# Kernel tuning notes

Measured on AMD Instinct MI355X. Metric: run time of the kernel, lower is better.

The kernel has to match this reference:

```python
import jax, jax.numpy as jnp
import numpy as np

HIDDEN = 512
BATCH = 64
SEQ = 1024
FUTURE = 16


def setup_inputs() -> dict:
    key = jax.random.key(0)
    ks = jax.random.split(key, 12)
    s = 0.05  # small init to keep the un-squashed LSTM recurrence stable
    H = HIDDEN
    inp = {
        "x": jax.random.normal(ks[0], (BATCH, SEQ), dtype=jnp.float32),
        # cell 1: input_length=1
        "W1": jax.random.normal(ks[1], (4 * H, 1), dtype=jnp.float32) * s,
        "bW1": jax.random.normal(ks[2], (4 * H,), dtype=jnp.float32) * s,
        "U1": jax.random.normal(ks[3], (4 * H, H), dtype=jnp.float32) * s,
        "bU1": jax.random.normal(ks[4], (4 * H,), dtype=jnp.float32) * s,
        # cell 2: input_length=H
        "W2": jax.random.normal(ks[5], (4 * H, H), dtype=jnp.float32) * s,
        "bW2": jax.random.normal(ks[6], (4 * H,), dtype=jnp.float32) * s,
        "U2": jax.random.normal(ks[7], (4 * H, H), dtype=jnp.float32) * s,
        "bU2": jax.random.normal(ks[8], (4 * H,), dtype=jnp.float32) * s,
        # output head: Linear(H, 1)
        "lw": jax.random.normal(ks[9], (1, H), dtype=jnp.float32) * s,
        "lb": jax.random.normal(ks[10], (1,), dtype=jnp.float32) * s,
        "future": FUTURE,
    }
    return inp


def _cell(x_t, h, c, W, bW, U, bU):
    # NOTE: faithful to source — NO sigmoid/tanh on the gates, only tanh on c_t.
    gates = x_t @ W.T + bW + h @ U.T + bU            # [B, 4H]
    i_t, f_t, g_t, o_t = jnp.split(gates, 4, axis=-1)
    c_t = f_t * c + i_t * g_t
    h_t = o_t * jnp.tanh(c_t)
    return h_t, c_t


def reference(x, W1, bW1, U1, bU1, W2, bW2, U2, bU2, lw, lb, future):
    B = x.shape[0]
    H = U1.shape[1]
    zeros = jnp.zeros((B, H), dtype=x.dtype)
    init = (zeros, zeros, zeros, zeros, jnp.zeros((B, 1), dtype=x.dtype))

    def run(carry, x_t):
        h1, c1, h2, c2, _ = carry
        h1, c1 = _cell(x_t, h1, c1, W1, bW1, U1, bU1)
        h2, c2 = _cell(h1, h2, c2, W2, bW2, U2, bU2)
        out = h2 @ lw.T + lb                          # [B, 1]
        return (h1, c1, h2, c2, out), out

    # teacher-forced pass over the observed sequence
    xs = x.T[:, :, None]                              # [T, B, 1]
    carry, outs = jax.lax.scan(run, init, xs)         # outs: [T, B, 1]

    if future > 0:
        def run_future(carry, _):
            return run(carry, carry[4])
        carry, outs_f = jax.lax.scan(run_future, carry, None, length=future)
        outs = jnp.concatenate([outs, outs_f], axis=0)

    return outs[:, :, 0].T                            # [B, T+future]
```

## Files before the change

kernel.cpp:

```cpp
#include <hip/hip_runtime.h>
#include <math.h>

#define HID 512
#define B 64
#define SEQT 1024
#define FUT 16
#define TT (SEQT + FUT)
#define NWG 256
#define TPB 512
#define NWAVE 8
#define JPW 2
#define HB (HID * B)
#define BLOBF 12288

#define WS_H1_F   512
#define WS_H2_F   (WS_H1_F + 2 * HB)
#define WS_BLOB_F (WS_H2_F + 2 * HB)
#define WS_XT_F   (WS_BLOB_F + NWG * BLOBF)
#define WS_TOT_F  (WS_XT_F + SEQT * B)

__device__ inline void pub_store(float* p, float v) {
  __hip_atomic_store(p, v, __ATOMIC_RELAXED, __HIP_MEMORY_SCOPE_AGENT);
}

__device__ inline void gbar4(int* bb, int wg, int bar) {
  __builtin_amdgcn_s_waitcnt(0);
  __syncthreads();
  const int tid  = threadIdx.x;
  const int lane = tid & 63;
  if (tid == 0) {
    __hip_atomic_store(bb + wg, bar, __ATOMIC_RELAXED, __HIP_MEMORY_SCOPE_AGENT);
    __builtin_amdgcn_fence(__ATOMIC_ACQUIRE, "agent");
  }
  if (wg == NWG - 1 && tid < 64) {
    for (;;) {
      int a = __hip_atomic_load(bb + lane,       __ATOMIC_RELAXED, __HIP_MEMORY_SCOPE_AGENT);
      int b = __hip_atomic_load(bb + 64  + lane, __ATOMIC_RELAXED, __HIP_MEMORY_SCOPE_AGENT);
      int c = __hip_atomic_load(bb + 128 + lane, __ATOMIC_RELAXED, __HIP_MEMORY_SCOPE_AGENT);
      int d = __hip_atomic_load(bb + 192 + lane, __ATOMIC_RELAXED, __HIP_MEMORY_SCOPE_AGENT);
      if (__all(a >= bar && b >= bar && c >= bar && d >= bar)) break;
      __builtin_amdgcn_s_sleep(2);
    }
    if (lane == 0)
      __hip_atomic_store(bb + 320, bar, __ATOMIC_RELAXED, __HIP_MEMORY_SCOPE_AGENT);
  }
  if (tid == 0) {
    while (__hip_atomic_load(bb + 320, __ATOMIC_RELAXED,
                             __HIP_MEMORY_SCOPE_AGENT) < bar) {
      __builtin_amdgcn_s_sleep(2);
    }
  }
  __syncthreads();
}

__global__ void __launch_bounds__(256) prep_ws(
    const float* __restrict__ x,
    const float* __restrict__ U1, const float* __restrict__ W2,
    const float* __restrict__ U2, float* __restrict__ ws)
{
  const int idx = blockIdx.x * blockDim.x + threadIdx.x;
  if (idx < WS_BLOB_F) {
    ws[idx] = 0.0f;
  }
  {
    const int i2 = idx - WS_BLOB_F;
    if (i2 >= 0 && i2 < NWG * BLOBF) {
      const int wg  = i2 / BLOBF;
      const int off = i2 - wg * BLOBF;
      const int j0  = wg * JPW;
      float v;
      if (off < 4096) {
        const int k = off >> 3, r = off & 7;
        const int row = (r >> 1) * HID + j0 + (r & 1);
        v = U1[(size_t)row * HID + k];
      } else {
        const int o2 = off - 4096;
        const int k = o2 >> 4, rr = o2 & 15;
        const int r = rr & 7;
        const int row = (r >> 1) * HID + j0 + (r & 1);
        v = (rr < 8) ? W2[(size_t)row * HID + k] : U2[(size_t)row * HID + k];
      }
      ws[WS_BLOB_F + i2] = v;
    }
  }
  {
    const int i3 = idx - WS_XT_F;
    if (i3 >= 0 && i3 < SEQT * B) {
      const int t = i3 >> 6, b = i3 & 63;
      ws[WS_XT_F + i3] = x[(size_t)b * SEQT + t];
    }
  }
}

__global__ void __launch_bounds__(TPB, 1) rnn_main(
    const float* __restrict__ W1, const float* __restrict__ bW1,
    const float* __restrict__ bU1,
    const float* __restrict__ bW2, const float* __restrict__ bU2,
    const float* __restrict__ lw, const float* __restrict__ lb,
    float* __restrict__ out,
    int* __restrict__ bb,
    float* __restrict__ h1b, float* __restrict__ h2b,
    const float* __restrict__ wbl, const float* __restrict__ xT)
{
  __shared__ float wlds[BLOBF];
  __shared__ float red[NWAVE][8][B];
  __shared__ float outred[NWAVE][B];
  __shared__ float c1s[JPW][B], c2s[JPW][B];
  __shared__ float w1c[8], bs1[8], bs2[8];

  const int wg   = blockIdx.x;
  const int j0   = wg * JPW;
  const int tid  = threadIdx.x;
  const int lane = tid & 63;
  const int wvu  = __builtin_amdgcn_readfirstlane(tid >> 6);

  {
    const float4* gsrc = (const float4*)(wbl + (size_t)wg * BLOBF);
    float4* ldst = (float4*)wlds;
    #pragma unroll
    for (int i = 0; i < BLOBF / 4 / TPB; ++i)
      ldst[i * TPB + tid] = gsrc[i * TPB + tid];
  }
  if (tid < JPW * B) { c1s[tid >> 6][lane] = 0.f; c2s[tid >> 6][lane] = 0.f; }
  if (tid < 8) {
    const int g = tid >> 1, jl = tid & 1;
    const int row = g * HID + j0 + jl;
    w1c[tid] = W1[row];
    bs1[tid] = bW1[row] + bU1[row];
    bs2[tid] = bW2[row] + bU2[row];
  }
  __syncthreads();

  const float* wl1 = wlds + wvu * 512;
  const float* wl2 = wlds + 4096 + wvu * 1024;
  const float lbv = lb[0];

  int bar = 0;
  for (int t = 0; t < TT; ++t) {
    const float* h1old = h1b + ((t + 1) & 1) * HB;
    float*       h1new = h1b + (t & 1) * HB;
    const float* h2old = h2b + ((t + 1) & 1) * HB;
    float*       h2new = h2b + (t & 1) * HB;

    float xvpref = 0.f;
    if (tid < JPW * B && t < SEQT) xvpref = xT[(size_t)t * B + lane];

    {
      const float4* hp = (const float4*)h1old + (size_t)(wvu * 16) * B + lane;
      float4 hq[16];
      #pragma unroll
      for (int i = 0; i < 16; ++i) hq[i] = hp[i * B];
      float a[8] = {0.f,0.f,0.f,0.f,0.f,0.f,0.f,0.f};
      #pragma unroll
      for (int c = 0; c < 16; ++c) {
        const float hh[4] = {hq[c].x, hq[c].y, hq[c].z, hq[c].w};
        #pragma unroll
        for (int j = 0; j < 4; ++j) {
          const float4 wA = *(const float4*)(wl1 + c * 32 + j * 8);
          const float4 wB = *(const float4*)(wl1 + c * 32 + j * 8 + 4);
          const float h = hh[j];
          a[0] = fmaf(wA.x, h, a[0]); a[1] = fmaf(wA.y, h, a[1]);
          a[2] = fmaf(wA.z, h, a[2]); a[3] = fmaf(wA.w, h, a[3]);
          a[4] = fmaf(wB.x, h, a[4]); a[5] = fmaf(wB.y, h, a[5]);
          a[6] = fmaf(wB.z, h, a[6]); a[7] = fmaf(wB.w, h, a[7]);
        }
      }
      #pragma unroll
      for (int r = 0; r < 8; ++r) red[wvu][r][lane] = a[r];
    }
    __syncthreads();

    if (tid < JPW * B) {
      const int jl = tid >> 6, b = tid & 63;
      const float xv = (t < SEQT) ? xvpref : out[(size_t)b * TT + (t - 1)];
      float gate[4];
      #pragma unroll
      for (int g = 0; g < 4; ++g) {
        const int r = g * 2 + jl;
        float s = bs1[r] + xv * w1c[r];
        #pragma unroll
        for (int w = 0; w < NWAVE; ++w) s += red[w][r][b];
        gate[g] = s;
      }
      const float c = gate[1] * c1s[jl][b] + gate[0] * gate[2];
      c1s[jl][b] = c;
      const int j = j0 + jl;
      pub_store(&h1new[(size_t)(j >> 2) * (B * 4) + b * 4 + (j & 3)],
                gate[3] * tanhf(c));
    }

    ++bar;
    gbar4(bb, wg, bar);

    if (wg == (t & 127) && t >= 1 && t <= SEQT - 1) {
      const float4* hb2 = (const float4*)h2old + (size_t)(wvu * 16) * B + lane;
      const float4* lw4 = (const float4*)lw + wvu * 16;
      float p = 0.f;
      #pragma unroll
      for (int i = 0; i < 16; ++i) {
        const float4 hv = hb2[i * B];
        const float4 wv = lw4[i];
        p = fmaf(wv.x, hv.x, p); p = fmaf(wv.y, hv.y, p);
        p = fmaf(wv.z, hv.z, p); p = fmaf(wv.w, hv.w, p);
      }
      outred[wvu][lane] = p;
      __syncthreads();
      if (tid < B) {
        float o = lbv;
        #pragma unroll
        for (int s = 0; s < NWAVE; ++s) o += outred[s][tid];
        pub_store(&out[(size_t)tid * TT + (t - 1)], o);
      }
      __syncthreads();
    }

    {
      const float4* pp4 = (const float4*)h1new + (size_t)(wvu * 16) * B + lane;
      const float4* qq4 = (const float4*)h2old + (size_t)(wvu * 16) * B + lane;
      float4 P[16], Q[16];
      #pragma unroll
      for (int i = 0; i < 16; ++i) P[i] = pp4[i * B];
      #pragma unroll
      for (int i = 0; i < 16; ++i) Q[i] = qq4[i * B];
      float a[8] = {0.f,0.f,0.f,0.f,0.f,0.f,0.f,0.f};
      #pragma unroll
      for (int c = 0; c < 16; ++c) {
        const float hp_[4] = {P[c].x, P[c].y, P[c].z, P[c].w};
        const float hq_[4] = {Q[c].x, Q[c].y, Q[c].z, Q[c].w};
        #pragma unroll
        for (int j = 0; j < 4; ++j) {
          const float4 w0 = *(const float4*)(wl2 + c * 64 + j * 16);
          const float4 w1 = *(const float4*)(wl2 + c * 64 + j * 16 + 4);
          const float4 w2 = *(const float4*)(wl2 + c * 64 + j * 16 + 8);
          const float4 w3 = *(const float4*)(wl2 + c * 64 + j * 16 + 12);
          const float hp1 = hp_[j], hq1 = hq_[j];
          a[0] = fmaf(w0.x, hp1, a[0]); a[1] = fmaf(w0.y, hp1, a[1]);
          a[2] = fmaf(w0.z, hp1, a[2]); a[3] = fmaf(w0.w, hp1, a[3]);
          a[4] = fmaf(w1.x, hp1, a[4]); a[5] = fmaf(w1.y, hp1, a[5]);
          a[6] = fmaf(w1.z, hp1, a[6]); a[7] = fmaf(w1.w, hp1, a[7]);
          a[0] = fmaf(w2.x, hq1, a[0]); a[1] = fmaf(w2.y, hq1, a[1]);
          a[2] = fmaf(w2.z, hq1, a[2]); a[3] = fmaf(w2.w, hq1, a[3]);
          a[4] = fmaf(w3.x, hq1, a[4]); a[5] = fmaf(w3.y, hq1, a[5]);
          a[6] = fmaf(w3.z, hq1, a[6]); a[7] = fmaf(w3.w, hq1, a[7]);
        }
      }
      #pragma unroll
      for (int r = 0; r < 8; ++r) red[wvu][r][lane] = a[r];
    }
    __syncthreads();

    if (tid < JPW * B) {
      const int jl = tid >> 6, b = tid & 63;
      float gate[4];
      #pragma unroll
      for (int g = 0; g < 4; ++g) {
        const int r = g * 2 + jl;
        float s = bs2[r];
        #pragma unroll
        for (int w = 0; w < NWAVE; ++w) s += red[w][r][b];
        gate[g] = s;
      }
      const float c = gate[1] * c2s[jl][b] + gate[0] * gate[2];
      c2s[jl][b] = c;
      const int j = j0 + jl;
      pub_store(&h2new[(size_t)(j >> 2) * (B * 4) + b * 4 + (j & 3)],
                gate[3] * tanhf(c));
    }
    __syncthreads();

    if (t >= SEQT - 1) {
      ++bar;
      gbar4(bb, wg, bar);
      if (wg == 0) {
        const float4* hb2 = (const float4*)h2new + (size_t)(wvu * 16) * B + lane;
        const float4* lw4 = (const float4*)lw + wvu * 16;
        float p = 0.f;
        #pragma unroll
        for (int i = 0; i < 16; ++i) {
          const float4 hv = hb2[i * B];
          const float4 wv = lw4[i];
          p = fmaf(wv.x, hv.x, p); p = fmaf(wv.y, hv.y, p);
          p = fmaf(wv.z, hv.z, p); p = fmaf(wv.w, hv.w, p);
        }
        outred[wvu][lane] = p;
        __syncthreads();
        if (tid < B) {
          float o = lbv;
          #pragma unroll
          for (int s = 0; s < NWAVE; ++s) o += outred[s][tid];
          pub_store(&out[(size_t)tid * TT + t], o);
        }
        __syncthreads();
      }
      ++bar;
      gbar4(bb, wg, bar);
    }
  }
}

__device__ inline void gbar(int* cnt, int target) {
  __syncthreads();
  if (threadIdx.x == 0) {
    __threadfence();
    __hip_atomic_fetch_add(cnt, 1, __ATOMIC_RELEASE, __HIP_MEMORY_SCOPE_AGENT);
    while (__hip_atomic_load(cnt, __ATOMIC_ACQUIRE, __HIP_MEMORY_SCOPE_AGENT) < target) {
      __builtin_amdgcn_s_sleep(2);
    }
  }
  __syncthreads();
}

__global__ void __launch_bounds__(TPB) zero_ws(float* ws, int n) {
  int i = blockIdx.x * blockDim.x + threadIdx.x;
  if (i < n) ws[i] = 0.0f;
}

__global__ void __launch_bounds__(TPB) rnn_fallback(
    const float* __restrict__ x,
    const float* __restrict__ W1, const float* __restrict__ bW1,
    const float* __restrict__ U1, const float* __restrict__ bU1,
    const float* __restrict__ W2, const float* __restrict__ bW2,
    const float* __restrict__ U2, const float* __restrict__ bU2,
    const float* __restrict__ lw, const float* __restrict__ lb,
    float* out, float* ws)
{
  __shared__ float red[NWAVE][8][B];
  __shared__ float outred[NWAVE][B];
  __shared__ float c1s[JPW][B], c2s[JPW][B];
  __shared__ float w1c[8], bs1[8], bs2[8];

  int* cnt   = (int*)ws;
  float* h1b = ws + 16;
  float* h2b = h1b + 2 * HB;

  const int wg   = blockIdx.x;
  const int j0   = wg * JPW;
  const int tid  = threadIdx.x;
  const int lane = tid & 63;
  const int wvu  = __builtin_amdgcn_readfirstlane(tid >> 6);
  const int kb   = wvu << 6;

  if (tid < JPW * B) { c1s[tid >> 6][lane] = 0.f; c2s[tid >> 6][lane] = 0.f; }
  if (tid < 8) {
    const int g = tid >> 1, jl = tid & 1;
    const int row = g * HID + j0 + jl;
    w1c[tid] = W1[row];
    bs1[tid] = bW1[row] + bU1[row];
    bs2[tid] = bW2[row] + bU2[row];
  }
  __syncthreads();

  const float* u1p[8]; const float* w2p[8]; const float* u2p[8];
  #pragma unroll
  for (int r = 0; r < 8; ++r) {
    const int row = (r >> 1) * HID + j0 + (r & 1);
    u1p[r] = U1 + (size_t)row * HID + kb;
    w2p[r] = W2 + (size_t)row * HID + kb;
    u2p[r] = U2 + (size_t)row * HID + kb;
  }
  const float lbv = lb[0];

  int bar = 0;
  for (int t = 0; t < TT; ++t) {
    const float* h1old = h1b + ((t + 1) & 1) * HB;
    float*       h1new = h1b + (t & 1) * HB;
    const float* h2old = h2b + ((t + 1) & 1) * HB;
    float*       h2new = h2b + (t & 1) * HB;

    {
      const float* hp = h1old + (size_t)kb * B;
      float a0=0.f,a1=0.f,a2=0.f,a3=0.f,a4=0.f,a5=0.f,a6=0.f,a7=0.f;
      #pragma unroll 8
      for (int k = 0; k < 64; ++k) {
        const float hv = hp[k * B + lane];
        a0 = fmaf(u1p[0][k], hv, a0); a1 = fmaf(u1p[1][k], hv, a1);
        a2 = fmaf(u1p[2][k], hv, a2); a3 = fmaf(u1p[3][k], hv, a3);
        a4 = fmaf(u1p[4][k], hv, a4); a5 = fmaf(u1p[5][k], hv, a5);
        a6 = fmaf(u1p[6][k], hv, a6); a7 = fmaf(u1p[7][k], hv, a7);
      }
      red[wvu][0][lane]=a0; red[wvu][1][lane]=a1; red[wvu][2][lane]=a2; red[wvu][3][lane]=a3;
      red[wvu][4][lane]=a4; red[wvu][5][lane]=a5; red[wvu][6][lane]=a6; red[wvu][7][lane]=a7;
    }
    __syncthreads();

    if (tid < JPW * B) {
      const int jl = tid >> 6, b = tid & 63;
      const float xv = (t < SEQT) ? x[(size_t)b * SEQT + t]
                                  : out[(size_t)b * TT + (t - 1)];
      float gate[4];
      #pragma unroll
      for (int g = 0; g < 4; ++g) {
        const int r = g * 2 + jl;
        float s = bs1[r] + xv * w1c[r];
        #pragma unroll
        for (int w = 0; w < NWAVE; ++w) s += red[w][r][b];
        gate[g] = s;
      }
      const float c = gate[1] * c1s[jl][b] + gate[0] * gate[2];
      c1s[jl][b] = c;
      h1new[(size_t)(j0 + jl) * B + b] = gate[3] * tanhf(c);
    }

    ++bar;
    gbar(cnt, NWG * bar);

    if (wg == 0 && t >= 1 && t <= SEQT - 1) {
      const float* hb2 = h2old + (size_t)(wvu * 64) * B;
      const float* lwp = lw + wvu * 64;
      float p = 0.f;
      #pragma unroll 8
      for (int j = 0; j < 64; ++j) p = fmaf(lwp[j], hb2[j * B + lane], p);
      outred[wvu][lane] = p;
      __syncthreads();
      if (tid < B) {
        float o = lbv;
        #pragma unroll
        for (int s = 0; s < NWAVE; ++s) o += outred[s][tid];
        out[(size_t)tid * TT + (t - 1)] = o;
      }
      __syncthreads();
    }

    {
      const float* h1p = h1new + (size_t)kb * B;
      const float* h2p = h2old + (size_t)kb * B;
      float s0=0.f,s1=0.f,s2=0.f,s3=0.f,s4=0.f,s5=0.f,s6=0.f,s7=0.f;
      float q0=0.f,q1=0.f,q2=0.f,q3=0.f,q4=0.f,q5=0.f,q6=0.f,q7=0.f;
      #pragma unroll 4
      for (int k = 0; k < 64; ++k) {
        const float h1v = h1p[k * B + lane];
        const float h2v = h2p[k * B + lane];
        s0 = fmaf(w2p[0][k], h1v, s0); q0 = fmaf(u2p[0][k], h2v, q0);
        s1 = fmaf(w2p[1][k], h1v, s1); q1 = fmaf(u2p[1][k], h2v, q1);
        s2 = fmaf(w2p[2][k], h1v, s2); q2 = fmaf(u2p[2][k], h2v, q2);
        s3 = fmaf(w2p[3][k], h1v, s3); q3 = fmaf(u2p[3][k], h2v, q3);
        s4 = fmaf(w2p[4][k], h1v, s4); q4 = fmaf(u2p[4][k], h2v, q4);
        s5 = fmaf(w2p[5][k], h1v, s5); q5 = fmaf(u2p[5][k], h2v, q5);
        s6 = fmaf(w2p[6][k], h1v, s6); q6 = fmaf(u2p[6][k], h2v, q6);
        s7 = fmaf(w2p[7][k], h1v, s7); q7 = fmaf(u2p[7][k], h2v, q7);
      }
      red[wvu][0][lane]=s0+q0; red[wvu][1][lane]=s1+q1;
      red[wvu][2][lane]=s2+q2; red[wvu][3][lane]=s3+q3;
      red[wvu][4][lane]=s4+q4; red[wvu][5][lane]=s5+q5;
      red[wvu][6][lane]=s6+q6; red[wvu][7][lane]=s7+q7;
    }
    __syncthreads();

    if (tid < JPW * B) {
      const int jl = tid >> 6, b = tid & 63;
      float gate[4];
      #pragma unroll
      for (int g = 0; g < 4; ++g) {
        const int r = g * 2 + jl;
        float s = bs2[r];
        #pragma unroll
        for (int w = 0; w < NWAVE; ++w) s += red[w][r][b];
        gate[g] = s;
      }
      const float c = gate[1] * c2s[jl][b] + gate[0] * gate[2];
      c2s[jl][b] = c;
      h2new[(size_t)(j0 + jl) * B + b] = gate[3] * tanhf(c);
    }
    __syncthreads();

    if (t >= SEQT - 1) {
      ++bar;
      gbar(cnt, NWG * bar);
      if (wg == 0) {
        const float* hb2 = h2new + (size_t)(wvu * 64) * B;
        const float* lwp = lw + wvu * 64;
        float p = 0.f;
        #pragma unroll 8
        for (int j = 0; j < 64; ++j) p = fmaf(lwp[j], hb2[j * B + lane], p);
        outred[wvu][lane] = p;
        __syncthreads();
        if (tid < B) {
          float o = lbv;
          #pragma unroll
          for (int s = 0; s < NWAVE; ++s) o += outred[s][tid];
          out[(size_t)tid * TT + t] = o;
        }
        __syncthreads();
      }
      ++bar;
      gbar(cnt, NWG * bar);
    }
  }
}

extern "C" void kernel_launch(void* const* d_in, const int* in_sizes, int n_in,
                              void* d_out, int out_size, void* d_ws, size_t ws_size,
                              hipStream_t stream) {
  (void)in_sizes; (void)n_in; (void)out_size;
  const float* x   = (const float*)d_in[0];
  const float* W1  = (const float*)d_in[1];
  const float* bW1 = (const float*)d_in[2];
  const float* U1  = (const float*)d_in[3];
  const float* bU1 = (const float*)d_in[4];
  const float* W2  = (const float*)d_in[5];
  const float* bW2 = (const float*)d_in[6];
  const float* U2  = (const float*)d_in[7];
  const float* bU2 = (const float*)d_in[8];
  const float* lw  = (const float*)d_in[9];
  const float* lb  = (const float*)d_in[10];

  float* out = (float*)d_out;
  float* ws  = (float*)d_ws;

  if (ws_size >= (size_t)WS_TOT_F * sizeof(float)) {
    prep_ws<<<(WS_TOT_F + 255) / 256, 256, 0, stream>>>(x, U1, W2, U2, ws);
    rnn_main<<<NWG, TPB, 0, stream>>>(W1, bW1, bU1, bW2, bU2, lw, lb, out,
                                      (int*)ws, ws + WS_H1_F, ws + WS_H2_F,
                                      ws + WS_BLOB_F, ws + WS_XT_F);
  } else {
    const int nzero = 16 + 4 * HID * B;
    zero_ws<<<(nzero + TPB - 1) / TPB, TPB, 0, stream>>>(ws, nzero);
    rnn_fallback<<<NWG, TPB, 0, stream>>>(x, W1, bW1, U1, bU1,
                                          W2, bW2, U2, bU2, lw, lb, out, ws);
  }
}
```

Measured before the change: 14.05 ms.

## Double main kernel threads to 1024 and keep h1 slice in registers across steps

Launches the persistent recurrence kernel with 16 waves per workgroup instead of 8, halving each wave's K-slice of the matvecs and the per-wave register arrays. The h1 values a wave loads for the layer-2 matvec are kept in registers and reused as the layer-1 recurrent input on the next timestep, removing one global reload of h1 per step. The cost is a wider reduction (16 partials per gate) and more threads taking part in each block sync, plus a larger reduction buffer in shared memory.

```diff
diff --git a/kernel.cpp b/kernel.cpp
--- a/kernel.cpp
+++ b/kernel.cpp
@@ -8,7 +8,8 @@
 #define TT (SEQT + FUT)
 #define NWG 256
 #define TPB 512
-#define NWAVE 8
+#define TPB1 1024
+#define NWAVE1 16
 #define JPW 2
 #define HB (HID * B)
 #define BLOBF 12288
@@ -92,7 +93,7 @@
   }
 }
 
-__global__ void __launch_bounds__(TPB, 1) rnn_main(
+__global__ void __launch_bounds__(TPB1, 1) rnn_main(
     const float* __restrict__ W1, const float* __restrict__ bW1,
     const float* __restrict__ bU1,
     const float* __restrict__ bW2, const float* __restrict__ bU2,
@@ -103,8 +104,8 @@
     const float* __restrict__ wbl, const float* __restrict__ xT)
 {
   __shared__ float wlds[BLOBF];
-  __shared__ float red[NWAVE][8][B];
-  __shared__ float outred[NWAVE][B];
+  __shared__ float red[NWAVE1][8][B];
+  __shared__ float outred[NWAVE1][B];
   __shared__ float c1s[JPW][B], c2s[JPW][B];
   __shared__ float w1c[8], bs1[8], bs2[8];
 
@@ -118,8 +119,8 @@
     const float4* gsrc = (const float4*)(wbl + (size_t)wg * BLOBF);
     float4* ldst = (float4*)wlds;
     #pragma unroll
-    for (int i = 0; i < BLOBF / 4 / TPB; ++i)
-      ldst[i * TPB + tid] = gsrc[i * TPB + tid];
+    for (int i = 0; i < BLOBF / 4 / TPB1; ++i)
+      ldst[i * TPB1 + tid] = gsrc[i * TPB1 + tid];
   }
   if (tid < JPW * B) { c1s[tid >> 6][lane] = 0.f; c2s[tid >> 6][lane] = 0.f; }
   if (tid < 8) {
@@ -131,13 +132,16 @@
   }
   __syncthreads();
 
-  const float* wl1 = wlds + wvu * 512;
-  const float* wl2 = wlds + 4096 + wvu * 1024;
+  const float* wl1 = wlds + wvu * 256;
+  const float* wl2 = wlds + 4096 + wvu * 512;
   const float lbv = lb[0];
+
+  float4 H1[8], Q[8];
+  #pragma unroll
+  for (int i = 0; i < 8; ++i) H1[i] = make_float4(0.f, 0.f, 0.f, 0.f);
 
   int bar = 0;
   for (int t = 0; t < TT; ++t) {
-    const float* h1old = h1b + ((t + 1) & 1) * HB;
     float*       h1new = h1b + (t & 1) * HB;
     const float* h2old = h2b + ((t + 1) & 1) * HB;
     float*       h2new = h2b + (t & 1) * HB;
@@ -146,14 +150,10 @@
     if (tid < JPW * B && t < SEQT) xvpref = xT[(size_t)t * B + lane];
 
     {
-      const float4* hp = (const float4*)h1old + (size_t)(wvu * 16) * B + lane;
-      float4 hq[16];
-      #pragma unroll
-      for (int i = 0; i < 16; ++i) hq[i] = hp[i * B];
       float a[8] = {0.f,0.f,0.f,0.f,0.f,0.f,0.f,0.f};
       #pragma unroll
-      for (int c = 0; c < 16; ++c) {
-        const float hh[4] = {hq[c].x, hq[c].y, hq[c].z, hq[c].w};
+      for (int c = 0; c < 8; ++c) {
+        const float hh[4] = {H1[c].x, H1[c].y, H1[c].z, H1[c].w};
         #pragma unroll
         for (int j = 0; j < 4; ++j) {
           const float4 wA = *(const float4*)(wl1 + c * 32 + j * 8);
@@ -179,7 +179,7 @@
         const int r = g * 2 + jl;
         float s = bs1[r] + xv * w1c[r];
         #pragma unroll
-        for (int w = 0; w < NWAVE; ++w) s += red[w][r][b];
+        for (int w = 0; w < NWAVE1; ++w) s += red[w][r][b];
         gate[g] = s;
       }
       const float c = gate[1] * c1s[jl][b] + gate[0] * gate[2];
@@ -193,11 +193,11 @@
     gbar4(bb, wg, bar);
 
     if (wg == (t & 127) && t >= 1 && t <= SEQT - 1) {
-      const float4* hb2 = (const float4*)h2old + (size_t)(wvu * 16) * B + lane;
-      const float4* lw4 = (const float4*)lw + wvu * 16;
+      const float4* hb2 = (const float4*)h2old + (size_t)(wvu * 8) * B + lane;
+      const float4* lw4 = (const float4*)lw + wvu * 8;
       float p = 0.f;
       #pragma unroll
-      for (int i = 0; i < 16; ++i) {
+      for (int i = 0; i < 8; ++i) {
         const float4 hv = hb2[i * B];
         const float4 wv = lw4[i];
         p = fmaf(wv.x, hv.x, p); p = fmaf(wv.y, hv.y, p);
@@ -208,24 +208,23 @@
       if (tid < B) {
         float o = lbv;
         #pragma unroll
-        for (int s = 0; s < NWAVE; ++s) o += outred[s][tid];
+        for (int s = 0; s < NWAVE1; ++s) o += outred[s][tid];
         pub_store(&out[(size_t)tid * TT + (t - 1)], o);
       }
       __syncthreads();
     }
 
     {
-      const float4* pp4 = (const float4*)h1new + (size_t)(wvu * 16) * B + lane;
-      const float4* qq4 = (const float4*)h2old + (size_t)(wvu * 16) * B + lane;
-      float4 P[16], Q[16];
-      #pragma unroll
-      for (int i = 0; i < 16; ++i) P[i] = pp4[i * B];
-      #pragma unroll
-      for (int i = 0; i < 16; ++i) Q[i] = qq4[i * B];
+      const float4* pp4 = (const float4*)h1new + (size_t)(wvu * 8) * B + lane;
+      const float4* qq4 = (const float4*)h2old + (size_t)(wvu * 8) * B + lane;
+      #pragma unroll
+      for (int i = 0; i < 8; ++i) H1[i] = pp4[i * B];
+      #pragma unroll
+      for (int i = 0; i < 8; ++i) Q[i] = qq4[i * B];
       float a[8] = {0.f,0.f,0.f,0.f,0.f,0.f,0.f,0.f};
       #pragma unroll
-      for (int c = 0; c < 16; ++c) {
-        const float hp_[4] = {P[c].x, P[c].y, P[c].z, P[c].w};
+      for (int c = 0; c < 8; ++c) {
+        const float hp_[4] = {H1[c].x, H1[c].y, H1[c].z, H1[c].w};
         const float hq_[4] = {Q[c].x, Q[c].y, Q[c].z, Q[c].w};
         #pragma unroll
         for (int j = 0; j < 4; ++j) {
@@ -257,7 +256,7 @@
         const int r = g * 2 + jl;
         float s = bs2[r];
         #pragma unroll
-        for (int w = 0; w < NWAVE; ++w) s += red[w][r][b];
+        for (int w = 0; w < NWAVE1; ++w) s += red[w][r][b];
         gate[g] = s;
       }
       const float c = gate[1] * c2s[jl][b] + gate[0] * gate[2];
@@ -272,11 +271,11 @@
       ++bar;
       gbar4(bb, wg, bar);
       if (wg == 0) {
-        const float4* hb2 = (const float4*)h2new + (size_t)(wvu * 16) * B + lane;
-        const float4* lw4 = (const float4*)lw + wvu * 16;
+        const float4* hb2 = (const float4*)h2new + (size_t)(wvu * 8) * B + lane;
+        const float4* lw4 = (const float4*)lw + wvu * 8;
         float p = 0.f;
         #pragma unroll
-        for (int i = 0; i < 16; ++i) {
+        for (int i = 0; i < 8; ++i) {
           const float4 hv = hb2[i * B];
           const float4 wv = lw4[i];
           p = fmaf(wv.x, hv.x, p); p = fmaf(wv.y, hv.y, p);
@@ -287,7 +286,7 @@
         if (tid < B) {
           float o = lbv;
           #pragma unroll
-          for (int s = 0; s < NWAVE; ++s) o += outred[s][tid];
+          for (int s = 0; s < NWAVE1; ++s) o += outred[s][tid];
           pub_store(&out[(size_t)tid * TT + t], o);
         }
         __syncthreads();
@@ -324,8 +323,8 @@
     const float* __restrict__ lw, const float* __restrict__ lb,
     float* out, float* ws)
 {
-  __shared__ float red[NWAVE][8][B];
-  __shared__ float outred[NWAVE][B];
+  __shared__ float red[8][8][B];
+  __shared__ float outred[8][B];
   __shared__ float c1s[JPW][B], c2s[JPW][B];
   __shared__ float w1c[8], bs1[8], bs2[8];
 
@@ -393,7 +392,7 @@
         const int r = g * 2 + jl;
         float s = bs1[r] + xv * w1c[r];
         #pragma unroll
-        for (int w = 0; w < NWAVE; ++w) s += red[w][r][b];
+        for (int w = 0; w < 8; ++w) s += red[w][r][b];
         gate[g] = s;
       }
       const float c = gate[1] * c1s[jl][b] + gate[0] * gate[2];
@@ -415,7 +414,7 @@
       if (tid < B) {
         float o = lbv;
         #pragma unroll
-        for (int s = 0; s < NWAVE; ++s) o += outred[s][tid];
+        for (int s = 0; s < 8; ++s) o += outred[s][tid];
         out[(size_t)tid * TT + (t - 1)] = o;
       }
       __syncthreads();
@@ -454,7 +453,7 @@
         const int r = g * 2 + jl;
         float s = bs2[r];
         #pragma unroll
-        for (int w = 0; w < NWAVE; ++w) s += red[w][r][b];
+        for (int w = 0; w < 8; ++w) s += red[w][r][b];
         gate[g] = s;
       }
       const float c = gate[1] * c2s[jl][b] + gate[0] * gate[2];
@@ -477,7 +476,7 @@
         if (tid < B) {
           float o = lbv;
           #pragma unroll
-          for (int s = 0; s < NWAVE; ++s) o += outred[s][tid];
+          for (int s = 0; s < 8; ++s) o += outred[s][tid];
           out[(size_t)tid * TT + t] = o;
         }
         __syncthreads();
@@ -509,9 +508,9 @@
 
   if (ws_size >= (size_t)WS_TOT_F * sizeof(float)) {
     prep_ws<<<(WS_TOT_F + 255) / 256, 256, 0, stream>>>(x, U1, W2, U2, ws);
-    rnn_main<<<NWG, TPB, 0, stream>>>(W1, bW1, bU1, bW2, bU2, lw, lb, out,
-                                      (int*)ws, ws + WS_H1_F, ws + WS_H2_F,
-                                      ws + WS_BLOB_F, ws + WS_XT_F);
+    rnn_main<<<NWG, TPB1, 0, stream>>>(W1, bW1, bU1, bW2, bU2, lw, lb, out,
+                                       (int*)ws, ws + WS_H1_F, ws + WS_H2_F,
+                                       ws + WS_BLOB_F, ws + WS_XT_F);
   } else {
     const int nzero = 16 + 4 * HID * B;
     zero_ws<<<(nzero + TPB - 1) / TPB, TPB, 0, stream>>>(ws, nzero);
```

After: 12.34 ms. 12.2% less time.
